# Kernel tuning notes

Hardware: AMD Instinct MI355X
Metric: run time of the kernel (lower is better)

The kernel has to match this reference:

```python
import jax, jax.numpy as jnp
import numpy as np

B, L, D_MODEL, H = 2, 2048, 2048, 16
HD = D_MODEL // H  # 128 head dim
EPS = 1e-6


def rms_norm(x, scale):
    # float32 RMSNorm over last dim, per Flux QKNorm
    x32 = x.astype(jnp.float32)
    rrms = jax.lax.rsqrt(jnp.mean(x32 * x32, axis=-1, keepdims=True) + EPS)
    return (x32 * rrms) * scale


def apply_rope(xq, xk, freqs_cis):
    # xq, xk: [B, L, H, D]; freqs_cis: [1, L, 1, D/2, 2, 2]
    shp = xq.shape
    xq_ = xq.astype(jnp.float32).reshape(*shp[:-1], -1, 1, 2)
    xk_ = xk.astype(jnp.float32).reshape(*shp[:-1], -1, 1, 2)
    xq_out = freqs_cis[..., 0] * xq_[..., 0] + freqs_cis[..., 1] * xq_[..., 1]
    xk_out = freqs_cis[..., 0] * xk_[..., 0] + freqs_cis[..., 1] * xk_[..., 1]
    return xq_out.reshape(shp).astype(xq.dtype), xk_out.reshape(shp).astype(xk.dtype)


def setup_inputs() -> dict:
    key = jax.random.key(0)
    k1, k2, k3, k4 = jax.random.split(key, 4)
    x = jax.random.normal(k1, (B, L, D_MODEL), dtype=jnp.float32)
    pe = jax.random.normal(k2, (1, L, 1, HD // 2, 2, 2), dtype=jnp.float32)
    w_qkv = jax.random.normal(k3, (D_MODEL, 3 * D_MODEL), dtype=jnp.float32) * (D_MODEL ** -0.5)
    w_proj = jax.random.normal(k4, (D_MODEL, D_MODEL), dtype=jnp.float32) * (D_MODEL ** -0.5)
    q_scale = jnp.ones((HD,), dtype=jnp.float32)
    k_scale = jnp.ones((HD,), dtype=jnp.float32)
    return {"x": x, "pe": pe, "w_qkv": w_qkv, "w_proj": w_proj,
            "q_scale": q_scale, "k_scale": k_scale}


def reference(x, pe, w_qkv, w_proj, q_scale, k_scale):
    qkv = x @ w_qkv                                  # [B, L, 3*H*D]
    qkv = qkv.reshape(B, L, 3, H, HD)
    q, k, v = qkv[:, :, 0], qkv[:, :, 1], qkv[:, :, 2]  # [B, L, H, D]
    # QK RMSNorm (cast back to v's dtype, per QKNorm.forward)
    q = rms_norm(q, q_scale).astype(v.dtype)
    k = rms_norm(k, k_scale).astype(v.dtype)
    # RoPE
    q, k = apply_rope(q, k, pe)
    # non-causal SDPA
    scale = HD ** -0.5
    scores = jnp.einsum('blhd,bmhd->bhlm', q, k) * scale
    attn = jax.nn.softmax(scores, axis=-1)
    out = jnp.einsum('bhlm,bmhd->blhd', attn, v)     # [B, L, H, D]
    out = out.reshape(B, L, H * HD)
    return out @ w_proj
```

## Files before the change

kernel.cpp:

```cpp
#include <hip/hip_runtime.h>

typedef unsigned short u16;
typedef __bf16 bf16x8 __attribute__((ext_vector_type(8)));
typedef float f32x4 __attribute__((ext_vector_type(4)));

#define DEV static __device__ __forceinline__

constexpr int Bc  = 2;
constexpr int Lc  = 2048;
constexpr int Dc  = 2048;
constexpr int Hc  = 16;
constexpr int HDc = 128;
constexpr int Mc  = Bc * Lc;
constexpr int N3c = 3 * Dc;

DEV u16 f2bf(float f) {
  unsigned u = __builtin_bit_cast(unsigned, f);
  u += 0x7fffu + ((u >> 16) & 1u);
  return (u16)(u >> 16);
}
DEV float bf2f(u16 h) { return __builtin_bit_cast(float, ((unsigned)h) << 16); }

DEV void load16(const void* g, void* l) {
  __builtin_amdgcn_global_load_lds(
      (__attribute__((address_space(1))) void*)(g),
      (__attribute__((address_space(3))) void*)(l), 16, 0, 0);
}

__global__ __launch_bounds__(256) void k_prep(const float* __restrict__ x,
                                              const float* __restrict__ w_qkv,
                                              const float* __restrict__ w_proj,
                                              u16* __restrict__ xb,
                                              u16* __restrict__ wqkvT,
                                              u16* __restrict__ wpT) {
  __shared__ u16 t[128 * 136];
  int bid = blockIdx.x;
  int tid = threadIdx.x;
  if (bid < 4096) {
    int i = bid * 256 + tid;
    const float4* s = (const float4*)x;
    float4 a = s[2 * i], b = s[2 * i + 1];
    uint4 o;
    o.x = f2bf(a.x) | ((unsigned)f2bf(a.y) << 16);
    o.y = f2bf(a.z) | ((unsigned)f2bf(a.w) << 16);
    o.z = f2bf(b.x) | ((unsigned)f2bf(b.y) << 16);
    o.w = f2bf(b.z) | ((unsigned)f2bf(b.w) << 16);
    ((uint4*)xb)[i] = o;
    return;
  }
  const float* src;
  u16* dst;
  int tiles_c;
  long ss;
  if (bid < 4096 + 768) {
    int bx = bid - 4096;
    src = w_qkv; dst = wqkvT; tiles_c = 48; ss = N3c;
    int tr = bx / tiles_c, tc = bx % tiles_c;
    src += (long)tr * 128 * ss + tc * 128;
    dst += (long)(tc * 128) * Dc + tr * 128;
  } else {
    int bx = bid - 4864;
    src = w_proj; dst = wpT; tiles_c = 16; ss = Dc;
    int tr = bx / tiles_c, tc = bx % tiles_c;
    src += (long)tr * 128 * ss + tc * 128;
    dst += (long)(tc * 128) * Dc + tr * 128;
  }
#pragma unroll
  for (int p = 0; p < 16; p++) {
    int r = p * 8 + (tid >> 5);
    int c4 = (tid & 31) * 4;
    float4 v = *(const float4*)(src + (long)r * ss + c4);
    t[(c4 + 0) * 136 + r] = f2bf(v.x);
    t[(c4 + 1) * 136 + r] = f2bf(v.y);
    t[(c4 + 2) * 136 + r] = f2bf(v.z);
    t[(c4 + 3) * 136 + r] = f2bf(v.w);
  }
  __syncthreads();
#pragma unroll
  for (int p = 0; p < 8; p++) {
    int c = p * 16 + (tid >> 4);
    int r8 = (tid & 15) * 8;
    uint4 v = *(const uint4*)&t[c * 136 + r8];
    *(uint4*)(dst + (long)c * Dc + r8) = v;
  }
}

__global__ __launch_bounds__(256) void k_vtrans(const u16* __restrict__ qkvb,
                                                u16* __restrict__ Vt) {
  int lt = blockIdx.x;
  int bh = blockIdx.y;
  int b = bh >> 4, h = bh & 15;
  const u16* s = qkvb + (long)(b * Lc + lt * 128) * N3c + 2 * Dc + h * HDc;
  u16* d = Vt + (long)bh * HDc * Lc + lt * 128;
  __shared__ u16 t[128 * 136];
  int tid = threadIdx.x;
#pragma unroll
  for (int p = 0; p < 8; p++) {
    int r = p * 16 + (tid >> 4);
    int c = (tid & 15) * 8;
    uint4 v = *(const uint4*)(s + (long)r * N3c + c);
    const u16* pv = (const u16*)&v;
#pragma unroll
    for (int j = 0; j < 8; j++) t[(c + j) * 136 + r] = pv[j];
  }
  __syncthreads();
#pragma unroll
  for (int p = 0; p < 8; p++) {
    int c = p * 16 + (tid >> 4);
    int r8 = (tid & 15) * 8;
    *(uint4*)(d + (long)c * Lc + r8) = *(const uint4*)&t[c * 136 + r8];
  }
}

DEV void cstore(float* p, float v) { *p = v; }
DEV void cstore(u16* p, float v) { *p = f2bf(v); }

template <typename OT>
__global__ __launch_bounds__(512, 2) void k_gemm2p(const u16* __restrict__ A,
                                                   const u16* __restrict__ Bt,
                                                   OT* __restrict__ C,
                                                   int M, int N, int K,
                                                   int RM, int RC) {
  __shared__ __align__(16) u16 sA[3][128 * 64];
  __shared__ __align__(16) u16 sB[3][256 * 64];

  int nb = N >> 8;
  int x = blockIdx.x & 7;
  int u = blockIdx.x >> 3;
  int rcr = nb / RC;
  int brow = (x / rcr) * RM + (u % RM);
  int bcol = (x % rcr) * RC + (u / RM);

  int tid = threadIdx.x, w = tid >> 6, lane = tid & 63;
  int wm = w >> 2, wn = w & 3;
  int quad = lane >> 4, l15 = lane & 15;
  int lr = lane >> 3, lc = lane & 7;
  int NT = K >> 6;

  const u16* Ag = A + (long)(brow * 128 + w * 8 + lr) * K + (lc ^ lr) * 8;
  const u16* Bg = Bt + (long)(bcol * 256 + w * 8 + lr) * K + (lc ^ lr) * 8;

  f32x4 acc[4][4] = {};
  bf16x8 a[4][2];
  bf16x8 b[4][2];

#define STAGE_A(c, t)                                                          \
  if ((t) < NT) {                                                              \
    _Pragma("unroll") for (int j = 0; j < 2; j++)                              \
        load16(Ag + (long)(j * 64) * K + (long)(t) * 64,                       \
               &sA[c][(j * 64 + w * 8) * 64]);                                 \
  }
#define STAGE_B(c, t)                                                          \
  if ((t) < NT) {                                                              \
    _Pragma("unroll") for (int j = 0; j < 4; j++)                              \
        load16(Bg + (long)(j * 64) * K + (long)(t) * 64,                       \
               &sB[c][(j * 64 + w * 8) * 64]);                                 \
  }
#define LDAB(c)                                                                \
  _Pragma("unroll") for (int mi = 0; mi < 4; mi++) {                           \
    int r = wm * 64 + mi * 16 + l15;                                           \
    _Pragma("unroll") for (int kk = 0; kk < 2; kk++)                           \
        a[mi][kk] =                                                            \
        *(const bf16x8*)&sA[c][r * 64 + (((kk * 4 + quad) ^ (r & 7)) << 3)];   \
  }                                                                            \
  _Pragma("unroll") for (int fi = 0; fi < 4; fi++) {                           \
    int rn = wn * 64 + fi * 16 + l15;                                          \
    _Pragma("unroll") for (int kk = 0; kk < 2; kk++)                           \
        b[fi][kk] =                                                            \
        *(const bf16x8*)&sB[c][rn * 64 + (((kk * 4 + quad) ^ (rn & 7)) << 3)]; \
  }
#define MFMAH(qm)                                                              \
  _Pragma("unroll") for (int mi = 0; mi < 2; mi++)                             \
  _Pragma("unroll") for (int fi = 0; fi < 4; fi++)                             \
  _Pragma("unroll") for (int kk = 0; kk < 2; kk++)                             \
      acc[(qm)*2 + mi][fi] = __builtin_amdgcn_mfma_f32_16x16x32_bf16(          \
          a[(qm)*2 + mi][kk], b[fi][kk], acc[(qm)*2 + mi][fi], 0, 0, 0);
#define BAR() __builtin_amdgcn_s_barrier()
#define LGKM0()                                      \
  asm volatile("s_waitcnt lgkmcnt(0)" ::: "memory"); \
  __builtin_amdgcn_sched_barrier(0)

#define TILE(c, t)                                                             \
  {                                                                            \
    LDAB(c);                                                                   \
    LGKM0();                                                                   \
    __builtin_amdgcn_s_setprio(1);                                             \
    MFMAH(0);                                                                  \
    __builtin_amdgcn_s_setprio(0);                                             \
    BAR();                        \
    STAGE_A(c, (t) + 3);                                                       \
    STAGE_B(c, (t) + 3);                                                       \
    __builtin_amdgcn_s_setprio(1);                                             \
    MFMAH(1);                                                                  \
    __builtin_amdgcn_s_setprio(0);                                             \
    if ((t) < NT - 3) {                                                        \
      asm volatile("s_waitcnt vmcnt(12)" ::: "memory");                        \
    } else if ((t) == NT - 3) {                                                \
      asm volatile("s_waitcnt vmcnt(6)" ::: "memory");                         \
    } else {                                                                   \
      asm volatile("s_waitcnt vmcnt(0)" ::: "memory");                         \
    }                                                                          \
    __builtin_amdgcn_sched_barrier(0);                                         \
    BAR();                          \
  }

  STAGE_A(0, 0);
  STAGE_B(0, 0);
  STAGE_A(1, 1);
  STAGE_B(1, 1);
  STAGE_A(2, 2);
  STAGE_B(2, 2);
  asm volatile("s_waitcnt vmcnt(12)" ::: "memory");
  __builtin_amdgcn_sched_barrier(0);
  BAR();

  int kt = 0;
  for (; kt + 2 < NT; kt += 3) {
    TILE(0, kt);
    TILE(1, kt + 1);
    TILE(2, kt + 2);
  }
  if (kt < NT) { TILE(0, kt); }
  if (kt + 1 < NT) { TILE(1, kt + 1); }

  long orow = (long)brow * 128 + wm * 64;
  int ocol = bcol * 256 + wn * 64;
#pragma unroll
  for (int mi = 0; mi < 4; mi++)
#pragma unroll
    for (int fi = 0; fi < 4; fi++)
#pragma unroll
      for (int r = 0; r < 4; r++)
        cstore(&C[(orow + mi * 16 + quad * 4 + r) * (long)N + ocol + fi * 16 + l15],
               acc[mi][fi][r]);
#undef STAGE_A
#undef STAGE_B
#undef LDAB
#undef MFMAH
#undef BAR
#undef LGKM0
#undef TILE
}

__global__ __launch_bounds__(256) void k_rmsrope(const u16* __restrict__ qkvb,
                                                 const float* __restrict__ pe,
                                                 const float* __restrict__ qsc,
                                                 const float* __restrict__ ksc,
                                                 u16* __restrict__ Qr,
                                                 u16* __restrict__ Kr) {
  int row = blockIdx.x;
  int l = row & (Lc - 1);
  int b = row >> 11;
  int tid = threadIdx.x;
  int h = tid >> 4, s16 = tid & 15;
  int d0 = s16 * 8;
  const u16* qp = qkvb + (long)row * N3c + h * HDc + d0;
  uint4 qv = *(const uint4*)qp;
  uint4 kv = *(const uint4*)(qp + Dc);
  const u16* qu = (const u16*)&qv;
  const u16* ku = (const u16*)&kv;
  float q[8], k[8];
#pragma unroll
  for (int j = 0; j < 8; j++) {
    q[j] = bf2f(qu[j]);
    k[j] = bf2f(ku[j]);
  }
  float sq = 0.f, sk = 0.f;
#pragma unroll
  for (int j = 0; j < 8; j++) {
    sq += q[j] * q[j];
    sk += k[j] * k[j];
  }
#pragma unroll
  for (int m = 1; m < 16; m <<= 1) {
    sq += __shfl_xor(sq, m);
    sk += __shfl_xor(sk, m);
  }
  float rq = rsqrtf(sq * (1.f / HDc) + 1e-6f);
  float rk = rsqrtf(sk * (1.f / HDc) + 1e-6f);
  float qs8[8], ks8[8];
  *(float4*)&qs8[0] = *(const float4*)(qsc + d0);
  *(float4*)&qs8[4] = *(const float4*)(qsc + d0 + 4);
  *(float4*)&ks8[0] = *(const float4*)(ksc + d0);
  *(float4*)&ks8[4] = *(const float4*)(ksc + d0 + 4);
#pragma unroll
  for (int j = 0; j < 8; j++) {
    q[j] *= rq * qs8[j];
    k[j] *= rk * ks8[j];
  }
  float e[16];
  const float* pep = pe + (long)l * 256 + s16 * 16;
#pragma unroll
  for (int j = 0; j < 4; j++) *(float4*)&e[j * 4] = *(const float4*)(pep + j * 4);
  float qo[8], ko[8];
#pragma unroll
  for (int p = 0; p < 4; p++) {
    float e00 = e[p * 4 + 0], e01 = e[p * 4 + 1];
    float e10 = e[p * 4 + 2], e11 = e[p * 4 + 3];
    qo[2 * p]     = e00 * q[2 * p] + e01 * q[2 * p + 1];
    qo[2 * p + 1] = e10 * q[2 * p] + e11 * q[2 * p + 1];
    ko[2 * p]     = e00 * k[2 * p] + e01 * k[2 * p + 1];
    ko[2 * p + 1] = e10 * k[2 * p] + e11 * k[2 * p + 1];
  }
  constexpr float RS = 0.08838834764831845f;
  uint4 oq, ok;
  oq.x = f2bf(qo[0] * RS) | ((unsigned)f2bf(qo[1] * RS) << 16);
  oq.y = f2bf(qo[2] * RS) | ((unsigned)f2bf(qo[3] * RS) << 16);
  oq.z = f2bf(qo[4] * RS) | ((unsigned)f2bf(qo[5] * RS) << 16);
  oq.w = f2bf(qo[6] * RS) | ((unsigned)f2bf(qo[7] * RS) << 16);
  ok.x = f2bf(ko[0]) | ((unsigned)f2bf(ko[1]) << 16);
  ok.y = f2bf(ko[2]) | ((unsigned)f2bf(ko[3]) << 16);
  ok.z = f2bf(ko[4]) | ((unsigned)f2bf(ko[5]) << 16);
  ok.w = f2bf(ko[6]) | ((unsigned)f2bf(ko[7]) << 16);
  long o = (((long)(b * Hc + h)) * Lc + l) * HDc + d0;
  *(uint4*)(Qr + o) = oq;
  *(uint4*)(Kr + o) = ok;
}

__global__ __launch_bounds__(256, 3) void k_attn(const u16* __restrict__ Qr,
                                                 const u16* __restrict__ Kr,
                                                 const u16* __restrict__ Vt,
                                                 u16* __restrict__ Ao) {
  __shared__ u16 smem[24576];
  u16* sQ = smem;
  u16* sK = smem + 8192;
  u16* sV = smem + 16384;
  u16* sP = sQ;
  int bx = blockIdx.x;
  int bh = (bx & 7) | ((bx >> 8) << 3);
  int lt = (bx >> 3) & 31;
  const u16* Qg = Qr + ((long)bh * Lc + lt * 64) * HDc;
  const u16* Kg = Kr + (long)bh * Lc * HDc;
  const u16* Vg = Vt + (long)bh * HDc * Lc;
  int tid = threadIdx.x, w = tid >> 6, lane = tid & 63;
  int quad = lane >> 4, l15 = lane & 15;
  int wsl = w >> 1, wsm = w & 1;
  int wd = w >> 1, wl2 = w & 1;

  int vrr0 = w * 8 + (lane >> 3);
  int vg0 = (lane & 7) ^ (vrr0 & 7);
  const u16* Vg0 = Vg + (long)(vrr0 + 0)  * Lc + vg0 * 8;
  const u16* Vg1 = Vg + (long)(vrr0 + 32) * Lc + vg0 * 8;
  const u16* Vg2 = Vg + (long)(vrr0 + 64) * Lc + vg0 * 8;
  const u16* Vg3 = Vg + (long)(vrr0 + 96) * Lc + vg0 * 8;
  u16* sVw = sV + (w * 8) * 64 + lane * 8;

#pragma unroll
  for (int i = 0; i < 4; i++) {
    int r = i * 16 + w * 4 + quad;
    int gch = l15 ^ (r & 15);
    load16(Qg + (long)r * HDc + gch * 8, sQ + (i * 16 + w * 4) * 128);
  }
  __syncthreads();
  bf16x8 qf[2][4];
#pragma unroll
  for (int mi = 0; mi < 2; mi++) {
    int l = wsl * 32 + mi * 16 + l15;
#pragma unroll
    for (int kk = 0; kk < 4; kk++)
      qf[mi][kk] = *(const bf16x8*)&sQ[l * 128 + (((kk * 4 + quad) ^ l15) << 3)];
  }

#pragma unroll
  for (int i = 0; i < 4; i++) {
    int r = i * 16 + w * 4 + quad;
    int gch = l15 ^ (r & 15);
    load16(Kg + (long)r * HDc + gch * 8, sK + (i * 16 + w * 4) * 128);
  }
  uint4 vr0 = *(const uint4*)(Vg0);
  uint4 vr1 = *(const uint4*)(Vg1);
  uint4 vr2 = *(const uint4*)(Vg2);
  uint4 vr3 = *(const uint4*)(Vg3);

  f32x4 o[4][2] = {};
  float rs[8] = {};
  for (int t = 0; t < 32; t++) {
    int m0 = t * 64;
    __syncthreads();
    *(uint4*)(sVw + 0 * 32 * 64) = vr0;
    *(uint4*)(sVw + 1 * 32 * 64) = vr1;
    *(uint4*)(sVw + 2 * 32 * 64) = vr2;
    *(uint4*)(sVw + 3 * 32 * 64) = vr3;
    __syncthreads();
    f32x4 s[2][2] = {};
#pragma unroll
    for (int kk = 0; kk < 4; kk++) {
      bf16x8 bk[2];
#pragma unroll
      for (int ni = 0; ni < 2; ni++) {
        int m = wsm * 32 + ni * 16 + l15;
        bk[ni] = *(const bf16x8*)&sK[m * 128 + (((kk * 4 + quad) ^ l15) << 3)];
      }
#pragma unroll
      for (int mi = 0; mi < 2; mi++)
#pragma unroll
        for (int ni = 0; ni < 2; ni++)
          s[mi][ni] =
              __builtin_amdgcn_mfma_f32_16x16x32_bf16(qf[mi][kk], bk[ni], s[mi][ni], 0, 0, 0);
    }
#pragma unroll
    for (int mi = 0; mi < 2; mi++)
#pragma unroll
      for (int ni = 0; ni < 2; ni++) {
        int pc = wsm * 32 + ni * 16 + l15;
#pragma unroll
        for (int r = 0; r < 4; r++) {
          int pr = wsl * 32 + mi * 16 + quad * 4 + r;
          float p = __expf(s[mi][ni][r]);
          rs[mi * 4 + r] += p;
          unsigned u = __builtin_bit_cast(unsigned, p) + 0x8000u;
          sP[pr * 64 + ((((pc >> 3) ^ (pr & 7)) << 3) | (pc & 7))] = (u16)(u >> 16);
        }
      }
    __syncthreads();
    if (t + 1 < 32) {
      int m1 = m0 + 64;
#pragma unroll
      for (int i = 0; i < 4; i++) {
        int r = i * 16 + w * 4 + quad;
        int gch = l15 ^ (r & 15);
        load16(Kg + ((long)(m1 + r)) * HDc + gch * 8, sK + (i * 16 + w * 4) * 128);
      }
      vr0 = *(const uint4*)(Vg0 + m1);
      vr1 = *(const uint4*)(Vg1 + m1);
      vr2 = *(const uint4*)(Vg2 + m1);
      vr3 = *(const uint4*)(Vg3 + m1);
    }
#pragma unroll
    for (int kk = 0; kk < 2; kk++) {
      bf16x8 av[4], bp[2];
#pragma unroll
      for (int mi = 0; mi < 4; mi++) {
        int d = wd * 64 + mi * 16 + l15;
        av[mi] = *(const bf16x8*)&sV[d * 64 + (((kk * 4 + quad) ^ (d & 7)) << 3)];
      }
#pragma unroll
      for (int ni = 0; ni < 2; ni++) {
        int l = wl2 * 32 + ni * 16 + l15;
        bp[ni] = *(const bf16x8*)&sP[l * 64 + (((kk * 4 + quad) ^ (l & 7)) << 3)];
      }
#pragma unroll
      for (int mi = 0; mi < 4; mi++)
#pragma unroll
        for (int ni = 0; ni < 2; ni++)
          o[mi][ni] =
              __builtin_amdgcn_mfma_f32_16x16x32_bf16(av[mi], bp[ni], o[mi][ni], 0, 0, 0);
    }
  }
  __syncthreads();
  float* red  = (float*)sK;
  float* rsum = (float*)sV;
#pragma unroll
  for (int mi = 0; mi < 2; mi++)
#pragma unroll
    for (int r = 0; r < 4; r++) {
      int l = wsl * 32 + mi * 16 + quad * 4 + r;
      red[l * 33 + wsm * 16 + l15] = rs[mi * 4 + r];
    }
  __syncthreads();
  if (tid < 64) {
    float a = 0.f;
#pragma unroll
    for (int j = 0; j < 32; j++) a += red[tid * 33 + j];
    rsum[tid] = a;
  }
  __syncthreads();
  int b = bh >> 4, h = bh & 15;
#pragma unroll
  for (int ni = 0; ni < 2; ni++) {
    int l = wl2 * 32 + ni * 16 + l15;
    float inv = 1.f / rsum[l];
    long rowb = ((long)(b * Lc + lt * 64 + l)) * Dc + h * HDc;
#pragma unroll
    for (int mi = 0; mi < 4; mi++) {
      int d = wd * 64 + mi * 16 + quad * 4;
      ushort4 pk;
      pk.x = f2bf(o[mi][ni][0] * inv);
      pk.y = f2bf(o[mi][ni][1] * inv);
      pk.z = f2bf(o[mi][ni][2] * inv);
      pk.w = f2bf(o[mi][ni][3] * inv);
      *(ushort4*)(Ao + rowb + d) = pk;
    }
  }
}

extern "C" void kernel_launch(void* const* d_in, const int* in_sizes, int n_in,
                              void* d_out, int out_size, void* d_ws, size_t ws_size,
                              hipStream_t stream) {
  const float* x      = (const float*)d_in[0];
  const float* pe     = (const float*)d_in[1];
  const float* w_qkv  = (const float*)d_in[2];
  const float* w_proj = (const float*)d_in[3];
  const float* qs     = (const float*)d_in[4];
  const float* ks     = (const float*)d_in[5];
  float* out = (float*)d_out;
  char* ws = (char*)d_ws;

  u16* xb    = (u16*)(ws);
  u16* wqkvT = (u16*)(ws + 16777216);
  u16* wpT   = (u16*)(ws + 41943040);
  u16* qkvb  = (u16*)(ws + 50331648);
  u16* Qr    = (u16*)(ws + 100663296);
  u16* Kr    = (u16*)(ws + 117440512);
  u16* Vtw   = (u16*)(ws + 134217728);
  u16* Ao    = (u16*)(ws + 150994944);

  k_prep<<<5120, 256, 0, stream>>>(x, w_qkv, w_proj, xb, wqkvT, wpT);
  k_gemm2p<u16><<<32 * 24, 512, 0, stream>>>(xb, wqkvT, qkvb, Mc, N3c, Dc, 16, 6);
  k_rmsrope<<<Mc, 256, 0, stream>>>(qkvb, pe, qs, ks, Qr, Kr);
  k_vtrans<<<dim3(16, 32), 256, 0, stream>>>(qkvb, Vtw);
  k_attn<<<32 * 32, 256, 0, stream>>>(Qr, Kr, Vtw, Ao);
  k_gemm2p<float><<<32 * 8, 512, 0, stream>>>(Ao, wpT, out, Mc, Dc, Dc, 8, 4);
}
```

Measured before the change: 408.4 us.

## Fuse QK RMSNorm, RoPE and V transpose into the QKV GEMM epilogue

The QKV GEMM epilogue now applies RMSNorm, scale and RoPE to the Q and K tiles and writes them straight into the head-major Qr/Kr layouts. V tiles are transposed through shared memory and written directly into Vt. This removes the intermediate qkvb write and re-read and two kernel launches. In exchange it adds a cross-wave reduction with __syncthreads, shared-memory staging and extra register pressure in the GEMM epilogue. The epilogue also reuses the sA/sB buffers after the main loop, which depends on the earlier barriers being correct.

Result: faster. 395.5 us (-3.2%).

```diff
diff --git a/kernel.cpp b/kernel.cpp
--- a/kernel.cpp
+++ b/kernel.cpp
@@ -85,42 +85,21 @@
   }
 }
 
-__global__ __launch_bounds__(256) void k_vtrans(const u16* __restrict__ qkvb,
-                                                u16* __restrict__ Vt) {
-  int lt = blockIdx.x;
-  int bh = blockIdx.y;
-  int b = bh >> 4, h = bh & 15;
-  const u16* s = qkvb + (long)(b * Lc + lt * 128) * N3c + 2 * Dc + h * HDc;
-  u16* d = Vt + (long)bh * HDc * Lc + lt * 128;
-  __shared__ u16 t[128 * 136];
-  int tid = threadIdx.x;
-#pragma unroll
-  for (int p = 0; p < 8; p++) {
-    int r = p * 16 + (tid >> 4);
-    int c = (tid & 15) * 8;
-    uint4 v = *(const uint4*)(s + (long)r * N3c + c);
-    const u16* pv = (const u16*)&v;
-#pragma unroll
-    for (int j = 0; j < 8; j++) t[(c + j) * 136 + r] = pv[j];
-  }
-  __syncthreads();
-#pragma unroll
-  for (int p = 0; p < 8; p++) {
-    int c = p * 16 + (tid >> 4);
-    int r8 = (tid & 15) * 8;
-    *(uint4*)(d + (long)c * Lc + r8) = *(const uint4*)&t[c * 136 + r8];
-  }
-}
-
 DEV void cstore(float* p, float v) { *p = v; }
 DEV void cstore(u16* p, float v) { *p = f2bf(v); }
 
-template <typename OT>
+template <typename OT, bool FUSE>
 __global__ __launch_bounds__(512, 2) void k_gemm2p(const u16* __restrict__ A,
                                                    const u16* __restrict__ Bt,
                                                    OT* __restrict__ C,
                                                    int M, int N, int K,
-                                                   int RM, int RC) {
+                                                   int RM, int RC,
+                                                   const float* __restrict__ pe,
+                                                   const float* __restrict__ qsc,
+                                                   const float* __restrict__ ksc,
+                                                   u16* __restrict__ Qr,
+                                                   u16* __restrict__ Kr,
+                                                   u16* __restrict__ Vt) {
   __shared__ __align__(16) u16 sA[3][128 * 64];
   __shared__ __align__(16) u16 sB[3][256 * 64];
 
@@ -225,14 +204,108 @@
 
   long orow = (long)brow * 128 + wm * 64;
   int ocol = bcol * 256 + wn * 64;
-#pragma unroll
-  for (int mi = 0; mi < 4; mi++)
-#pragma unroll
-    for (int fi = 0; fi < 4; fi++)
-#pragma unroll
-      for (int r = 0; r < 4; r++)
-        cstore(&C[(orow + mi * 16 + quad * 4 + r) * (long)N + ocol + fi * 16 + l15],
-               acc[mi][fi][r]);
+  if constexpr (!FUSE) {
+#pragma unroll
+    for (int mi = 0; mi < 4; mi++)
+#pragma unroll
+      for (int fi = 0; fi < 4; fi++)
+#pragma unroll
+        for (int r = 0; r < 4; r++)
+          cstore(&C[(orow + mi * 16 + quad * 4 + r) * (long)N + ocol + fi * 16 + l15],
+                 acc[mi][fi][r]);
+  } else {
+    u16* ep = (u16*)sB + w * (64 * 72);
+    int lane8 = lane >> 3, c8 = (lane & 7) * 8;
+    if (bcol >= 16) {
+#pragma unroll
+      for (int mi = 0; mi < 4; mi++)
+#pragma unroll
+        for (int fi = 0; fi < 4; fi++)
+#pragma unroll
+          for (int r = 0; r < 4; r++)
+            ep[(fi * 16 + l15) * 72 + mi * 16 + quad * 4 + r] = f2bf(acc[mi][fi][r]);
+      asm volatile("s_waitcnt lgkmcnt(0)" ::: "memory");
+      __builtin_amdgcn_sched_barrier(0);
+      int h = ((bcol - 16) << 1) | (wn >> 1);
+      int bb = (int)(orow >> 11);
+      int lbase = (int)(orow & 2047);
+      long vbase = ((long)(bb * Hc + h) * HDc + (wn & 1) * 64) * Lc + lbase;
+#pragma unroll
+      for (int p = 0; p < 8; p++) {
+        int dl = p * 8 + lane8;
+        uint4 vv = *(const uint4*)&ep[dl * 72 + c8];
+        *(uint4*)(Vt + vbase + (long)dl * Lc + c8) = vv;
+      }
+    } else {
+      bool isQ = (bcol < 8);
+      float ss[4][4];
+#pragma unroll
+      for (int mi = 0; mi < 4; mi++)
+#pragma unroll
+        for (int r = 0; r < 4; r++) {
+          float s = 0.f;
+#pragma unroll
+          for (int fi = 0; fi < 4; fi++) s += acc[mi][fi][r] * acc[mi][fi][r];
+#pragma unroll
+          for (int m = 1; m < 16; m <<= 1) s += __shfl_xor(s, m);
+          ss[mi][r] = s;
+        }
+      float* red = (float*)sA;
+      if (l15 == 0) {
+#pragma unroll
+        for (int mi = 0; mi < 4; mi++)
+#pragma unroll
+          for (int r = 0; r < 4; r++)
+            red[(wm * 64 + mi * 16 + quad * 4 + r) * 4 + wn] = ss[mi][r];
+      }
+      __syncthreads();
+      float rr[4][4];
+#pragma unroll
+      for (int mi = 0; mi < 4; mi++)
+#pragma unroll
+        for (int r = 0; r < 4; r++) {
+          float tot = ss[mi][r] + red[(wm * 64 + mi * 16 + quad * 4 + r) * 4 + (wn ^ 1)];
+          rr[mi][r] = rsqrtf(tot * (1.f / HDc) + 1e-6f);
+        }
+      const float* scp = isQ ? qsc : ksc;
+      int dh = (wn & 1) * 64;
+      float sc[4];
+#pragma unroll
+      for (int fi = 0; fi < 4; fi++) sc[fi] = scp[dh + fi * 16 + l15];
+      constexpr float RS = 0.08838834764831845f;
+      float oscale = isQ ? RS : 1.f;
+      int dpar = l15 & 1;
+      int lg0 = (int)(orow & 2047);
+#pragma unroll
+      for (int mi = 0; mi < 4; mi++)
+#pragma unroll
+        for (int fi = 0; fi < 4; fi++) {
+          int d = dh + fi * 16 + l15;
+          const float* pb = pe + ((d >> 1) << 2) + ((d & 1) << 1);
+#pragma unroll
+          for (int r = 0; r < 4; r++) {
+            int lloc = mi * 16 + quad * 4 + r;
+            float v = acc[mi][fi][r] * rr[mi][r] * sc[fi];
+            float vp = __shfl_xor(v, 1);
+            float2 e = *(const float2*)(pb + (long)(lg0 + lloc) * 256);
+            float o = dpar ? (e.x * vp + e.y * v) : (e.x * v + e.y * vp);
+            ep[lloc * 72 + fi * 16 + l15] = f2bf(o * oscale);
+          }
+        }
+      asm volatile("s_waitcnt lgkmcnt(0)" ::: "memory");
+      __builtin_amdgcn_sched_barrier(0);
+      int h = isQ ? ((bcol << 1) | (wn >> 1)) : (((bcol - 8) << 1) | (wn >> 1));
+      u16* dst = isQ ? Qr : Kr;
+      int bb = (int)(orow >> 11);
+      long qbase = ((long)(bb * Hc + h) * Lc + lg0) * HDc + dh;
+#pragma unroll
+      for (int p = 0; p < 8; p++) {
+        int rl = p * 8 + lane8;
+        uint4 vv = *(const uint4*)&ep[rl * 72 + c8];
+        *(uint4*)(dst + qbase + (long)rl * HDc + c8) = vv;
+      }
+    }
+  }
 #undef STAGE_A
 #undef STAGE_B
 #undef LDAB
@@ -240,81 +313,6 @@
 #undef BAR
 #undef LGKM0
 #undef TILE
-}
-
-__global__ __launch_bounds__(256) void k_rmsrope(const u16* __restrict__ qkvb,
-                                                 const float* __restrict__ pe,
-                                                 const float* __restrict__ qsc,
-                                                 const float* __restrict__ ksc,
-                                                 u16* __restrict__ Qr,
-                                                 u16* __restrict__ Kr) {
-  int row = blockIdx.x;
-  int l = row & (Lc - 1);
-  int b = row >> 11;
-  int tid = threadIdx.x;
-  int h = tid >> 4, s16 = tid & 15;
-  int d0 = s16 * 8;
-  const u16* qp = qkvb + (long)row * N3c + h * HDc + d0;
-  uint4 qv = *(const uint4*)qp;
-  uint4 kv = *(const uint4*)(qp + Dc);
-  const u16* qu = (const u16*)&qv;
-  const u16* ku = (const u16*)&kv;
-  float q[8], k[8];
-#pragma unroll
-  for (int j = 0; j < 8; j++) {
-    q[j] = bf2f(qu[j]);
-    k[j] = bf2f(ku[j]);
-  }
-  float sq = 0.f, sk = 0.f;
-#pragma unroll
-  for (int j = 0; j < 8; j++) {
-    sq += q[j] * q[j];
-    sk += k[j] * k[j];
-  }
-#pragma unroll
-  for (int m = 1; m < 16; m <<= 1) {
-    sq += __shfl_xor(sq, m);
-    sk += __shfl_xor(sk, m);
-  }
-  float rq = rsqrtf(sq * (1.f / HDc) + 1e-6f);
-  float rk = rsqrtf(sk * (1.f / HDc) + 1e-6f);
-  float qs8[8], ks8[8];
-  *(float4*)&qs8[0] = *(const float4*)(qsc + d0);
-  *(float4*)&qs8[4] = *(const float4*)(qsc + d0 + 4);
-  *(float4*)&ks8[0] = *(const float4*)(ksc + d0);
-  *(float4*)&ks8[4] = *(const float4*)(ksc + d0 + 4);
-#pragma unroll
-  for (int j = 0; j < 8; j++) {
-    q[j] *= rq * qs8[j];
-    k[j] *= rk * ks8[j];
-  }
-  float e[16];
-  const float* pep = pe + (long)l * 256 + s16 * 16;
-#pragma unroll
-  for (int j = 0; j < 4; j++) *(float4*)&e[j * 4] = *(const float4*)(pep + j * 4);
-  float qo[8], ko[8];
-#pragma unroll
-  for (int p = 0; p < 4; p++) {
-    float e00 = e[p * 4 + 0], e01 = e[p * 4 + 1];
-    float e10 = e[p * 4 + 2], e11 = e[p * 4 + 3];
-    qo[2 * p]     = e00 * q[2 * p] + e01 * q[2 * p + 1];
-    qo[2 * p + 1] = e10 * q[2 * p] + e11 * q[2 * p + 1];
-    ko[2 * p]     = e00 * k[2 * p] + e01 * k[2 * p + 1];
-    ko[2 * p + 1] = e10 * k[2 * p] + e11 * k[2 * p + 1];
-  }
-  constexpr float RS = 0.08838834764831845f;
-  uint4 oq, ok;
-  oq.x = f2bf(qo[0] * RS) | ((unsigned)f2bf(qo[1] * RS) << 16);
-  oq.y = f2bf(qo[2] * RS) | ((unsigned)f2bf(qo[3] * RS) << 16);
-  oq.z = f2bf(qo[4] * RS) | ((unsigned)f2bf(qo[5] * RS) << 16);
-  oq.w = f2bf(qo[6] * RS) | ((unsigned)f2bf(qo[7] * RS) << 16);
-  ok.x = f2bf(ko[0]) | ((unsigned)f2bf(ko[1]) << 16);
-  ok.y = f2bf(ko[2]) | ((unsigned)f2bf(ko[3]) << 16);
-  ok.z = f2bf(ko[4]) | ((unsigned)f2bf(ko[5]) << 16);
-  ok.w = f2bf(ko[6]) | ((unsigned)f2bf(ko[7]) << 16);
-  long o = (((long)(b * Hc + h)) * Lc + l) * HDc + d0;
-  *(uint4*)(Qr + o) = oq;
-  *(uint4*)(Kr + o) = ok;
 }
 
 __global__ __launch_bounds__(256, 3) void k_attn(const u16* __restrict__ Qr,
@@ -506,9 +504,10 @@
   u16* Ao    = (u16*)(ws + 150994944);
 
   k_prep<<<5120, 256, 0, stream>>>(x, w_qkv, w_proj, xb, wqkvT, wpT);
-  k_gemm2p<u16><<<32 * 24, 512, 0, stream>>>(xb, wqkvT, qkvb, Mc, N3c, Dc, 16, 6);
-  k_rmsrope<<<Mc, 256, 0, stream>>>(qkvb, pe, qs, ks, Qr, Kr);
-  k_vtrans<<<dim3(16, 32), 256, 0, stream>>>(qkvb, Vtw);
+  k_gemm2p<u16, true><<<32 * 24, 512, 0, stream>>>(
+      xb, wqkvT, qkvb, Mc, N3c, Dc, 16, 6, pe, qs, ks, Qr, Kr, Vtw);
   k_attn<<<32 * 32, 256, 0, stream>>>(Qr, Kr, Vtw, Ao);
-  k_gemm2p<float><<<32 * 8, 512, 0, stream>>>(Ao, wpT, out, Mc, Dc, Dc, 8, 4);
+  k_gemm2p<float, false><<<32 * 8, 512, 0, stream>>>(
+      Ao, wpT, out, Mc, Dc, Dc, 8, 4, nullptr, nullptr, nullptr, nullptr, nullptr,
+      nullptr);
 }
```
